# Optimization experiments

Hardware: AMD Instinct MI355X
Metric: run time of the kernel (lower is better)

## Reference

```python
import jax, jax.numpy as jnp
import numpy as np

G = 8          # GroupNorm groups
EPS = 1e-5
L = 4          # num_layers
C = 64         # hidden_channels
CIN = 2        # in_channels


def group_norm(x, gamma, beta):
    B, Cc, H, W = x.shape
    xr = x.reshape(B, G, Cc // G, H, W)
    mu = xr.mean(axis=(2, 3, 4), keepdims=True)
    var = xr.var(axis=(2, 3, 4), keepdims=True)
    xn = ((xr - mu) * jax.lax.rsqrt(var + EPS)).reshape(B, Cc, H, W)
    return xn * gamma[:, None, None] + beta[:, None, None]


def conv1x1(x, w, b):
    # x: [B,Ci,H,W], w: [Co,Ci] -> [B,Co,H,W]
    return jnp.einsum('bchw,oc->bohw', x, w) + b[None, :, None, None]


def conv3x3(x, w, b):
    y = jax.lax.conv_general_dilated(x, w, (1, 1), 'SAME',
                                     dimension_numbers=('NCHW', 'OIHW', 'NCHW'))
    return y + b[None, :, None, None]


def setup_inputs() -> dict:
    key = jax.random.key(0)
    ks = jax.random.split(key, 20)
    s = 0.05
    inp = {
        'x': jax.random.normal(ks[0], (2, CIN, 256, 256), jnp.float32),
        'hidden': jnp.zeros((2, L, C, C), jnp.float32),
        'W_in': jax.random.normal(ks[1], (C, CIN, 3, 3), jnp.float32) * s,
        'b_in': jnp.zeros((C,), jnp.float32),
        'gamma': jnp.ones((L, C), jnp.float32),
        'beta': jnp.zeros((L, C), jnp.float32),
        'Wq': jax.random.normal(ks[2], (L, C, C), jnp.float32) * s,
        'bq': jnp.zeros((L, C), jnp.float32),
        'Wk': jax.random.normal(ks[3], (L, C, C), jnp.float32) * s,
        'bk': jnp.zeros((L, C), jnp.float32),
        'Wv': jax.random.normal(ks[4], (L, C, C), jnp.float32) * s,
        'bv': jnp.zeros((L, C), jnp.float32),
        'Wg': jax.random.normal(ks[5], (L, 2 * C, C), jnp.float32) * s,
        'bg': jnp.zeros((L, 2 * C), jnp.float32),
        'Wp': jax.random.normal(ks[6], (L, C, C), jnp.float32) * s,
        'bp': jnp.zeros((L, C), jnp.float32),
        'W_out': jax.random.normal(ks[7], (CIN, C, 3, 3), jnp.float32) * s,
        'b_out': jnp.zeros((CIN,), jnp.float32),
    }
    return inp


def gla_layer(feat, prev_mem, gamma, beta, Wq, bq, Wk, bk, Wv, bv, Wg, bg, Wp, bp):
    B, Cc, H, W = feat.shape
    N = H * W
    scale = Cc ** (-0.5)
    xn = group_norm(feat, gamma, beta)
    q = conv1x1(xn, Wq, bq).reshape(B, Cc, N) * scale
    k = conv1x1(xn, Wk, bk).reshape(B, Cc, N)
    v = conv1x1(xn, Wv, bv).reshape(B, Cc, N)
    gates = conv1x1(xn, Wg, bg).reshape(B, 2 * Cc, N)
    f_gate = jax.nn.sigmoid(gates[:, :Cc])
    i_gate = jax.nn.sigmoid(gates[:, Cc:])
    k_gated = k * i_gate
    new_knowledge = jnp.einsum('bcn,bdn->bcd', k_gated, v) / N  # [B,C,C]
    global_forget = f_gate.mean(axis=2)[:, :, None]              # [B,C,1]
    new_mem = global_forget * prev_mem + new_knowledge
    retrieved = jnp.einsum('bcn,bcd->bdn', q, new_mem).reshape(B, Cc, H, W)
    out = conv1x1(retrieved, Wp, bp) + feat
    return out, new_mem


def reference(x, hidden, W_in, b_in, gamma, beta, Wq, bq, Wk, bk, Wv, bv,
              Wg, bg, Wp, bp, W_out, b_out):
    feat = conv3x3(x, W_in, b_in)
    mems = []
    for i in range(L):
        feat, m = gla_layer(feat, hidden[:, i], gamma[i], beta[i],
                            Wq[i], bq[i], Wk[i], bk[i], Wv[i], bv[i],
                            Wg[i], bg[i], Wp[i], bp[i])
        mems.append(m)
    new_hidden = jnp.stack(mems, axis=1)  # [B,L,C,C]
    out = conv3x3(feat, W_out, b_out) + x
    return out, new_hidden
```

## Files before the change

kernel.cpp:

```cpp
#include <hip/hip_runtime.h>
#include <hip/hip_bf16.h>

typedef __hip_bfloat16 bf16;
typedef __attribute__((ext_vector_type(8))) short bf16x8;
typedef __attribute__((ext_vector_type(4))) short short4v;
typedef __attribute__((ext_vector_type(4))) float f32x4;

#define BATCH 2
#define CH 64
#define NPIX 65536
#define HDIM 256
#define NLAYER 4
#define NGRP 8
#define NSLOT 512

#define OFS_FEAT   0ull
#define OFS_KSLOT  33554432ull
#define OFS_MEMBG  50331648ull
#define OFS_FSUM   50348032ull
#define OFS_SSUM   50364416ull
#define OFS_BEFF   50380800ull
#define OFS_MEFFB  50381312ull
#define OFS_WKB    50397696ull
#define OFS_WVB    50430464ull
#define OFS_WGB    50463232ull
#define OFS_WTOUT  50528768ull
#define OFS_WPB    50533376ull
#define OFS_WQTB   50566144ull
#define ZERO_BYTES 32768

__device__ __forceinline__ float sigmoidf_(float x){ return 1.0f/(1.0f+__expf(-x)); }

__device__ __forceinline__ short f2bs(float x){
  unsigned u = __float_as_uint(x);
  u += 0x7fffu + ((u >> 16) & 1u);
  return (short)(u >> 16);
}

__device__ __forceinline__ float waveReduce(float v){
  #pragma unroll
  for (int off=32; off; off>>=1) v += __shfl_xor(v, off, 64);
  return v;
}

__global__ void k_prepw(const float* __restrict__ Wk, const float* __restrict__ Wv,
                        const float* __restrict__ Wg, const float* __restrict__ Wout,
                        const float* __restrict__ Wp, const float* __restrict__ Wq,
                        short* __restrict__ Wkb, short* __restrict__ Wvb,
                        short* __restrict__ Wgb, float* __restrict__ wtout,
                        short* __restrict__ Wpb, short* __restrict__ Wqtb){
  int i = blockIdx.x*256 + threadIdx.x;
  if (i < 16384){
    Wkb[i] = f2bs(Wk[i]);
    Wvb[i] = f2bs(Wv[i]);
    Wpb[i] = f2bs(Wp[i]);
    int l = i >> 12, within = i & 4095;
    int e = within >> 6, c = within & 63;
    Wqtb[i] = f2bs(Wq[l*4096 + c*64 + e]);
  }
  if (i < 32768) Wgb[i] = f2bs(Wg[i]);
  if (i < 1152){
    int o = i / 576, rem = i % 576;
    int k = rem >> 6, c = rem & 63;
    wtout[(o*9 + k)*64 + c] = Wout[o*576 + c*9 + k];
  }
}

__device__ __forceinline__ void blockStats(const float* gs, const float* gq,
                                           float* ssum_b, int t){
  __shared__ float sacc[16];
  if (t < 16) sacc[t] = 0.f;
  __syncthreads();
  #pragma unroll
  for (int g=0; g<NGRP; g++){
    float s  = waveReduce(gs[g]);
    float sq = waveReduce(gq[g]);
    if ((t & 63) == 0){ atomicAdd(&sacc[g*2], s); atomicAdd(&sacc[g*2+1], sq); }
  }
  __syncthreads();
  if (t < 16) atomicAdd(&ssum_b[t*32], sacc[t]);
}

__global__ void k_conv_in(const float* __restrict__ x, const float* __restrict__ w,
                          const float* __restrict__ bias,
                          float* __restrict__ feat, float* __restrict__ ssum){
  int b = blockIdx.y;
  int t = threadIdx.x;
  int n = blockIdx.x*256 + t;
  int y = n >> 8, xx = n & 255;
  float patch[18];
  int idx = 0;
  #pragma unroll
  for (int ci=0; ci<2; ci++)
    #pragma unroll
    for (int dy=-1; dy<=1; dy++)
      #pragma unroll
      for (int dx=-1; dx<=1; dx++){
        int yy = y+dy, xc = xx+dx;
        float v = 0.f;
        if (yy>=0 && yy<HDIM && xc>=0 && xc<HDIM)
          v = x[((b*2+ci)*HDIM + yy)*HDIM + xc];
        patch[idx++] = v;
      }
  float gs[NGRP], gq[NGRP];
  #pragma unroll
  for (int g=0; g<NGRP; g++){ gs[g]=0.f; gq[g]=0.f; }
  float* fb = feat + ((size_t)b*NPIX + n)*64;
  #pragma unroll
  for (int c4=0; c4<16; c4++){
    f32x4 ov;
    #pragma unroll
    for (int j=0;j<4;j++){
      int o = c4*4 + j;
      float acc = bias[o];
      #pragma unroll
      for (int k=0; k<18; k++) acc += w[o*18+k]*patch[k];
      ov[j] = acc;
      gs[o>>3] += acc; gq[o>>3] += acc*acc;
    }
    *(f32x4*)(fb + c4*4) = ov;
  }
  blockStats(gs, gq, ssum + b*512, t);
}

__device__ __forceinline__ void gnCoef(const float* __restrict__ ssum_l, int b, int t,
                                       const float* __restrict__ gammaP,
                                       const float* __restrict__ betaP, int l,
                                       float* s_gnA, float* s_gnB){
  if (t < 64){
    int g = t >> 3;
    const float inv = 1.0f/(8.0f*NPIX);
    float s  = ssum_l[(b*16 + g*2)*32];
    float sq = ssum_l[(b*16 + g*2 + 1)*32];
    float mu = s*inv;
    float var = sq*inv - mu*mu;
    float rstd = rsqrtf(var + 1e-5f);
    float A = rstd * gammaP[l*64 + t];
    s_gnA[t] = A;
    s_gnB[t] = betaP[l*64 + t] - mu * A;
  }
}

__global__ __launch_bounds__(256,3) void k_qkvg_know(
    const float* __restrict__ feat, const float* __restrict__ ssum_l,
    const float* __restrict__ gammaP, const float* __restrict__ betaP,
    const short* __restrict__ Wkb, const float* __restrict__ bkP,
    const short* __restrict__ Wvb, const float* __restrict__ bvP,
    const short* __restrict__ Wgb, const float* __restrict__ bgP,
    int l, float* __restrict__ kslot, float* __restrict__ f_sum)
{
  int b = blockIdx.y;
  int n0 = blockIdx.x * 128;
  int t = threadIdx.x;
  int w = t >> 6;
  int lane = t & 63;
  int m = lane & 15;
  int quad = lane >> 4;
  int rowbase = w*16;

  __shared__ short s_buf[17408];
  short* s_kg = s_buf;
  short* s_v  = s_buf + 8704;
  short* s_xn = s_buf;
  __shared__ float s_gnA[64], s_gnB[64];

  gnCoef(ssum_l, b, t, gammaP, betaP, l, s_gnA, s_gnB);

  float bkv[4], biv[4], bvv[4], bfv[4], fs[4];
  #pragma unroll
  for (int r=0;r<4;r++){
    int row = rowbase + quad*4 + r;
    bkv[r] = bkP[l*64 + row];
    biv[r] = bgP[l*128 + 64 + row];
    bvv[r] = bvP[l*64 + row];
    bfv[r] = bgP[l*128 + row];
    fs[r] = 0.f;
  }
  f32x4 z4 = {0.f,0.f,0.f,0.f};
  f32x4 accn[4];
  #pragma unroll
  for (int dt=0;dt<4;dt++) accn[dt] = z4;

  __syncthreads();

  const float* fbase = feat + ((size_t)b*NPIX + n0)*64;
  #pragma unroll
  for (int i=0;i<8;i++){
    int chunk = t + i*256;
    int px = chunk >> 4, cq = chunk & 15;
    f32x4 fv = *(const f32x4*)(fbase + px*64 + cq*4);
    short4v xs;
    #pragma unroll
    for (int j=0;j<4;j++)
      xs[j] = f2bs(fmaf(fv[j], s_gnA[cq*4+j], s_gnB[cq*4+j]));
    *(short4v*)&s_xn[px*72 + cq*4] = xs;
  }
  __syncthreads();

  bf16x8 Bf[2][8];
  #pragma unroll
  for (int kc=0;kc<2;kc++)
    #pragma unroll
    for (int nt=0;nt<8;nt++)
      Bf[kc][nt] = *(const bf16x8*)&s_xn[(nt*16+m)*72 + kc*32 + quad*8];
  __syncthreads();

  {
    bf16x8 Ak[2], Ai[2];
    #pragma unroll
    for (int kc=0;kc<2;kc++){
      Ak[kc] = *(const bf16x8*)&Wkb[l*4096 + (rowbase+m)*64 + kc*32 + quad*8];
      Ai[kc] = *(const bf16x8*)&Wgb[l*8192 + (64+rowbase+m)*64 + kc*32 + quad*8];
    }
    #pragma unroll
    for (int half=0; half<2; half++){
      f32x4 acck[4], acci[4];
      #pragma unroll
      for (int q4=0;q4<4;q4++){ acck[q4]=z4; acci[q4]=z4; }
      #pragma unroll
      for (int kc=0;kc<2;kc++)
        #pragma unroll
        for (int q4=0;q4<4;q4++){
          acck[q4] = __builtin_amdgcn_mfma_f32_16x16x32_bf16(Ak[kc], Bf[kc][half*4+q4], acck[q4], 0,0,0);
          acci[q4] = __builtin_amdgcn_mfma_f32_16x16x32_bf16(Ai[kc], Bf[kc][half*4+q4], acci[q4], 0,0,0);
        }
      #pragma unroll
      for (int q4=0;q4<4;q4++){
        int nt = half*4+q4;
        #pragma unroll
        for (int r=0;r<4;r++){
          int row = rowbase + quad*4 + r;
          float kv = acck[q4][r] + bkv[r];
          float iv = acci[q4][r] + biv[r];
          s_kg[row*136 + nt*16 + m] = f2bs(kv * sigmoidf_(iv));
        }
      }
    }
  }
  {
    bf16x8 Av[2];
    #pragma unroll
    for (int kc=0;kc<2;kc++)
      Av[kc] = *(const bf16x8*)&Wvb[l*4096 + (rowbase+m)*64 + kc*32 + quad*8];
    #pragma unroll
    for (int half=0; half<2; half++){
      f32x4 accv[4];
      #pragma unroll
      for (int q4=0;q4<4;q4++) accv[q4]=z4;
      #pragma unroll
      for (int kc=0;kc<2;kc++)
        #pragma unroll
        for (int q4=0;q4<4;q4++)
          accv[q4] = __builtin_amdgcn_mfma_f32_16x16x32_bf16(Av[kc], Bf[kc][half*4+q4], accv[q4], 0,0,0);
      #pragma unroll
      for (int q4=0;q4<4;q4++){
        int nt = half*4+q4;
        #pragma unroll
        for (int r=0;r<4;r++){
          int row = rowbase + quad*4 + r;
          s_v[row*136 + nt*16 + m] = f2bs(accv[q4][r] + bvv[r]);
        }
      }
    }
  }
  {
    bf16x8 Af[2];
    #pragma unroll
    for (int kc=0;kc<2;kc++)
      Af[kc] = *(const bf16x8*)&Wgb[l*8192 + (rowbase+m)*64 + kc*32 + quad*8];
    #pragma unroll
    for (int half=0; half<2; half++){
      f32x4 accf[4];
      #pragma unroll
      for (int q4=0;q4<4;q4++) accf[q4]=z4;
      #pragma unroll
      for (int kc=0;kc<2;kc++)
        #pragma unroll
        for (int q4=0;q4<4;q4++)
          accf[q4] = __builtin_amdgcn_mfma_f32_16x16x32_bf16(Af[kc], Bf[kc][half*4+q4], accf[q4], 0,0,0);
      #pragma unroll
      for (int q4=0;q4<4;q4++)
        #pragma unroll
        for (int r=0;r<4;r++)
          fs[r] += sigmoidf_(accf[q4][r] + bfv[r]);
    }
  }
  __syncthreads();

  #pragma unroll
  for (int kc4=0; kc4<4; kc4++){
    bf16x8 a = *(const bf16x8*)&s_kg[(rowbase + m)*136 + kc4*32 + quad*8];
    #pragma unroll
    for (int dt=0; dt<4; dt++){
      bf16x8 bv8 = *(const bf16x8*)&s_v[(dt*16 + m)*136 + kc4*32 + quad*8];
      accn[dt] = __builtin_amdgcn_mfma_f32_16x16x32_bf16(a, bv8, accn[dt], 0,0,0);
    }
  }

  #pragma unroll
  for (int off=1; off<16; off<<=1)
    #pragma unroll
    for (int r=0;r<4;r++) fs[r] += __shfl_xor(fs[r], off, 64);
  if (m == 0){
    #pragma unroll
    for (int r=0;r<4;r++)
      atomicAdd(&f_sum[(b*64 + rowbase + quad*4 + r)*32], fs[r]);
  }
  float* kr = kslot + ((size_t)b*NSLOT + blockIdx.x)*4096;
  #pragma unroll
  for (int dt=0;dt<4;dt++)
    #pragma unroll
    for (int r=0;r<4;r++)
      kr[(rowbase + quad*4 + r)*64 + dt*16 + m] = accn[dt][r];
}

__global__ __launch_bounds__(256) void k_memreduce(
    const float* __restrict__ kslot, const float* __restrict__ f_sum,
    const float* __restrict__ hidden_in, int l,
    float* __restrict__ hidden_out, short* __restrict__ membG)
{
  int b = blockIdx.y;
  int t = threadIdx.x;
  int e = t & 127;
  int half = t >> 7;
  int cd = blockIdx.x*128 + e;

  const float* base = kslot + ((size_t)b*NSLOT + half*256)*4096 + cd;
  float s = 0.f;
  #pragma unroll 16
  for (int sl=0; sl<256; sl++) s += base[(size_t)sl*4096];

  __shared__ float red[128];
  if (half) red[e] = s;
  __syncthreads();
  if (!half){
    const float invN = 1.0f/(float)NPIX;
    float kn = (s + red[e]) * invN;
    float fmean = f_sum[(b*64 + (cd>>6))*32] * invN;
    float pm = hidden_in[(size_t)(b*NLAYER+l)*4096 + cd];
    float nm = fmean*pm + kn;
    hidden_out[(size_t)(b*NLAYER+l)*4096 + cd] = nm;
    membG[b*4096 + cd] = f2bs(nm);
  }
}

__global__ __launch_bounds__(256) void k_meff(
    const short* __restrict__ membG, float* __restrict__ f_sum,
    const short* __restrict__ Wpb, const short* __restrict__ Wqtb,
    const float* __restrict__ bqP, const float* __restrict__ bpP,
    int l, short* __restrict__ Meffb, float* __restrict__ beff,
    float* __restrict__ ssum_next)
{
  int b = blockIdx.x;
  int t = threadIdx.x;
  int w = t >> 6;
  int lane = t & 63;
  int m = lane & 15;
  int quad = lane >> 4;

  __shared__ short s_memb[64*72];
  __shared__ short s_mfb[64*72];
  __shared__ float s_bq[64];

  if (t < 64) s_bq[t] = bqP[l*64 + t];

  #pragma unroll
  for (int i=0;i<16;i++){
    int cd = t + i*256;
    int c = cd >> 6, d = cd & 63;
    s_memb[c*72 + d] = membG[b*4096 + cd];
  }
  __syncthreads();
  if (t < 64) f_sum[(b*64 + t)*32] = 0.f;
  if (t < 16) ssum_next[(b*16 + t)*32] = 0.f;

  f32x4 z4 = {0.f,0.f,0.f,0.f};

  bf16x8 Ap[2];
  #pragma unroll
  for (int kc=0;kc<2;kc++)
    Ap[kc] = *(const bf16x8*)&Wpb[l*4096 + (w*16+m)*64 + kc*32 + quad*8];

  float be[4];
  #pragma unroll
  for (int r=0;r<4;r++) be[r] = 0.f;

  #pragma unroll
  for (int ct=0; ct<4; ct++){
    f32x4 a = z4;
    #pragma unroll
    for (int kc=0;kc<2;kc++){
      bf16x8 Bm = *(const bf16x8*)&s_memb[(ct*16+m)*72 + kc*32 + quad*8];
      a = __builtin_amdgcn_mfma_f32_16x16x32_bf16(Ap[kc], Bm, a, 0,0,0);
    }
    int c = ct*16 + m;
    #pragma unroll
    for (int r=0;r<4;r++){
      int o = w*16 + quad*4 + r;
      s_mfb[o*72 + c] = f2bs(a[r]);
      be[r] += a[r] * s_bq[c];
    }
  }
  #pragma unroll
  for (int off=1; off<16; off<<=1)
    #pragma unroll
    for (int r=0;r<4;r++) be[r] += __shfl_xor(be[r], off, 64);
  if (m == 0){
    #pragma unroll
    for (int r=0;r<4;r++){
      int o = w*16 + quad*4 + r;
      beff[b*64 + o] = bpP[l*64 + o] + 0.125f*be[r];
    }
  }
  __syncthreads();

  bf16x8 Am2[2];
  #pragma unroll
  for (int kc=0;kc<2;kc++)
    Am2[kc] = *(const bf16x8*)&s_mfb[(w*16+m)*72 + kc*32 + quad*8];
  #pragma unroll
  for (int et=0; et<4; et++){
    f32x4 a = z4;
    #pragma unroll
    for (int kc=0;kc<2;kc++){
      bf16x8 Bq = *(const bf16x8*)&Wqtb[l*4096 + (et*16+m)*64 + kc*32 + quad*8];
      a = __builtin_amdgcn_mfma_f32_16x16x32_bf16(Am2[kc], Bq, a, 0,0,0);
    }
    #pragma unroll
    for (int r=0;r<4;r++){
      int o = w*16 + quad*4 + r;
      Meffb[(size_t)b*4096 + o*64 + et*16 + m] = f2bs(0.125f*a[r]);
    }
  }
}

__global__ __launch_bounds__(256,3) void k_retrproj(
    const float* __restrict__ ssum_l,
    const float* __restrict__ gammaP, const float* __restrict__ betaP,
    const short* __restrict__ Meffb, const float* __restrict__ beff,
    int l, float* __restrict__ feat, float* __restrict__ ssum_next)
{
  int b = blockIdx.y;
  int n0 = blockIdx.x * 128;
  int t = threadIdx.x;
  int w = t >> 6;
  int lane = t & 63;
  int m = lane & 15;
  int quad = lane >> 4;

  __shared__ float s_out[128*68];
  short* s_xn = (short*)s_out;
  __shared__ float s_gnA[64], s_gnB[64], s_beff[64];
  __shared__ float s_sacc[16];

  gnCoef(ssum_l, b, t, gammaP, betaP, l, s_gnA, s_gnB);
  if (t < 64) s_beff[t] = beff[b*64 + t];
  if (t < 16) s_sacc[t] = 0.f;
  __syncthreads();

  const float* fbase = feat + ((size_t)b*NPIX + n0)*64;
  #pragma unroll
  for (int i=0;i<8;i++){
    int chunk = t + i*256;
    int px = chunk >> 4, cq = chunk & 15;
    f32x4 fv = *(const f32x4*)(fbase + px*64 + cq*4);
    short4v xs;
    #pragma unroll
    for (int j=0;j<4;j++)
      xs[j] = f2bs(fmaf(fv[j], s_gnA[cq*4+j], s_gnB[cq*4+j]));
    *(short4v*)&s_xn[px*72 + cq*4] = xs;
  }
  __syncthreads();

  bf16x8 Bf[2][8];
  #pragma unroll
  for (int kc=0;kc<2;kc++)
    #pragma unroll
    for (int nt=0;nt<8;nt++)
      Bf[kc][nt] = *(const bf16x8*)&s_xn[(nt*16+m)*72 + kc*32 + quad*8];

  bf16x8 Am[2];
  #pragma unroll
  for (int kc=0;kc<2;kc++)
    Am[kc] = *(const bf16x8*)&Meffb[(size_t)b*4096 + (w*16 + m)*64 + kc*32 + quad*8];
  __syncthreads();

  f32x4 acc[8];
  f32x4 z4 = {0.f,0.f,0.f,0.f};
  #pragma unroll
  for (int nt=0;nt<8;nt++) acc[nt]=z4;
  #pragma unroll
  for (int kc=0;kc<2;kc++)
    #pragma unroll
    for (int nt=0;nt<8;nt++)
      acc[nt] = __builtin_amdgcn_mfma_f32_16x16x32_bf16(Am[kc], Bf[kc][nt], acc[nt], 0,0,0);

  #pragma unroll
  for (int nt=0;nt<8;nt++)
    #pragma unroll
    for (int r=0;r<4;r++)
      s_out[(nt*16+m)*68 + w*16 + quad*4 + r] = acc[nt][r];
  __syncthreads();

  float gsv = 0.f, gqv = 0.f;
  int cq = t & 15;
  #pragma unroll
  for (int i=0;i<8;i++){
    int chunk = t + i*256;
    int px = chunk >> 4;
    float* fp = (float*)(fbase + px*64 + cq*4);
    f32x4 fv = *(const f32x4*)fp;
    f32x4 ov = *(const f32x4*)&s_out[px*68 + cq*4];
    f32x4 res;
    #pragma unroll
    for (int j=0;j<4;j++){
      float o = fv[j] + ov[j] + s_beff[cq*4+j];
      res[j] = o;
      gsv += o; gqv += o*o;
    }
    *(f32x4*)fp = res;
  }
  gsv += __shfl_xor(gsv, 1, 64);  gqv += __shfl_xor(gqv, 1, 64);
  gsv += __shfl_xor(gsv, 16, 64); gqv += __shfl_xor(gqv, 16, 64);
  gsv += __shfl_xor(gsv, 32, 64); gqv += __shfl_xor(gqv, 32, 64);
  if ((lane & 49) == 0){
    int g = (lane & 15) >> 1;
    atomicAdd(&s_sacc[g*2], gsv);
    atomicAdd(&s_sacc[g*2+1], gqv);
  }
  __syncthreads();
  if (t < 16) atomicAdd(&ssum_next[(b*16 + t)*32], s_sacc[t]);
}

__global__ void k_conv_out(const float* __restrict__ feat, const float* __restrict__ wt,
                           const float* __restrict__ bias,
                           const float* __restrict__ xin, float* __restrict__ out){
  int b = blockIdx.y;
  int y = blockIdx.x;
  int xx = threadIdx.x;
  float acc0 = bias[0], acc1 = bias[1];
  #pragma unroll
  for (int dy=-1; dy<=1; dy++){
    int yy = y + dy;
    if (yy < 0 || yy >= HDIM) continue;
    #pragma unroll
    for (int dx=-1; dx<=1; dx++){
      int xc = xx + dx;
      if (xc >= 0 && xc < HDIM){
        const float* fp = feat + ((size_t)b*NPIX + yy*HDIM + xc)*64;
        const float* w0 = wt + ((0*3 + dy+1)*3 + dx+1)*64;
        const float* w1 = wt + ((1*3 + dy+1)*3 + dx+1)*64;
        #pragma unroll
        for (int c4=0;c4<16;c4++){
          f32x4 fv  = *(const f32x4*)(fp + c4*4);
          f32x4 wv0 = *(const f32x4*)(w0 + c4*4);
          f32x4 wv1 = *(const f32x4*)(w1 + c4*4);
          #pragma unroll
          for (int j=0;j<4;j++){
            acc0 += fv[j]*wv0[j];
            acc1 += fv[j]*wv1[j];
          }
        }
      }
    }
  }
  size_t p0 = (size_t)(b*2+0)*NPIX + y*HDIM + xx;
  size_t p1 = (size_t)(b*2+1)*NPIX + y*HDIM + xx;
  out[p0] = acc0 + xin[p0];
  out[p1] = acc1 + xin[p1];
}

extern "C" void kernel_launch(void* const* d_in, const int* in_sizes, int n_in,
                              void* d_out, int out_size, void* d_ws, size_t ws_size,
                              hipStream_t stream){
  char* ws = (char*)d_ws;
  float* feat  = (float*)(ws + OFS_FEAT);
  float* kslot = (float*)(ws + OFS_KSLOT);
  short* membg = (short*)(ws + OFS_MEMBG);
  float* fsum  = (float*)(ws + OFS_FSUM);
  float* ssum  = (float*)(ws + OFS_SSUM);
  float* beff  = (float*)(ws + OFS_BEFF);
  short* meffb = (short*)(ws + OFS_MEFFB);
  short* wkb   = (short*)(ws + OFS_WKB);
  short* wvb   = (short*)(ws + OFS_WVB);
  short* wgb   = (short*)(ws + OFS_WGB);
  float* wtout = (float*)(ws + OFS_WTOUT);
  short* wpb   = (short*)(ws + OFS_WPB);
  short* wqtb  = (short*)(ws + OFS_WQTB);

  const float* x      = (const float*)d_in[0];
  const float* hidden = (const float*)d_in[1];
  const float* W_in   = (const float*)d_in[2];
  const float* b_in   = (const float*)d_in[3];
  const float* gamma  = (const float*)d_in[4];
  const float* beta   = (const float*)d_in[5];
  const float* Wq     = (const float*)d_in[6];
  const float* bq     = (const float*)d_in[7];
  const float* Wk     = (const float*)d_in[8];
  const float* bk     = (const float*)d_in[9];
  const float* Wv     = (const float*)d_in[10];
  const float* bv     = (const float*)d_in[11];
  const float* Wg     = (const float*)d_in[12];
  const float* bg     = (const float*)d_in[13];
  const float* Wp     = (const float*)d_in[14];
  const float* bp     = (const float*)d_in[15];
  const float* W_out  = (const float*)d_in[16];
  const float* b_out  = (const float*)d_in[17];

  float* out        = (float*)d_out;
  float* hidden_out = out + BATCH*2*NPIX;

  hipMemsetAsync(ws + OFS_FSUM, 0, ZERO_BYTES, stream);
  k_prepw<<<dim3(128), dim3(256), 0, stream>>>(Wk, Wv, Wg, W_out, Wp, Wq,
                                               wkb, wvb, wgb, wtout, wpb, wqtb);
  k_conv_in<<<dim3(HDIM, BATCH), dim3(256), 0, stream>>>(x, W_in, b_in, feat, ssum);

  for (int l=0; l<NLAYER; l++){
    float* ssum_l = ssum + (l & 1)*1024;
    float* ssum_n = ssum + ((l+1) & 1)*1024;
    k_qkvg_know<<<dim3(NPIX/128, BATCH), dim3(256), 0, stream>>>(
        feat, ssum_l, gamma, beta, wkb, bk, wvb, bv, wgb, bg, l, kslot, fsum);
    k_memreduce<<<dim3(32, BATCH), dim3(256), 0, stream>>>(
        kslot, fsum, hidden, l, hidden_out, membg);
    k_meff<<<dim3(BATCH), dim3(256), 0, stream>>>(
        membg, fsum, wpb, wqtb, bq, bp, l, meffb, beff, ssum_n);
    k_retrproj<<<dim3(NPIX/128, BATCH), dim3(256), 0, stream>>>(
        ssum_l, gamma, beta, meffb, beff, l, feat, ssum_n);
  }

  k_conv_out<<<dim3(HDIM, BATCH), dim3(256), 0, stream>>>(feat, wtout, b_out, x, out);
}
```

Baseline: 393.0 us.

## Store per-block knowledge partials as bf16 and fuse memreduce with meff

Per-block C×C knowledge partials are now written as bf16 instead of fp32, which halves the scratch traffic between the projection kernel and the reduction. The reduction and the effective-matrix kernels are merged into one launch. An atomic counter per layer and batch lets the last-finishing block do the Meff computation. This removes one kernel launch per layer and the traffic cost of the partials, at the price of bf16 rounding in the partial sums and reliance on a threadfence and counter pattern.

Result: slower. 409.9 us (+4.3%).

```diff
diff --git a/kernel.cpp b/kernel.cpp
--- a/kernel.cpp
+++ b/kernel.cpp
@@ -16,18 +16,19 @@
 
 #define OFS_FEAT   0ull
 #define OFS_KSLOT  33554432ull
-#define OFS_MEMBG  50331648ull
-#define OFS_FSUM   50348032ull
-#define OFS_SSUM   50364416ull
-#define OFS_BEFF   50380800ull
-#define OFS_MEFFB  50381312ull
-#define OFS_WKB    50397696ull
-#define OFS_WVB    50430464ull
-#define OFS_WGB    50463232ull
-#define OFS_WTOUT  50528768ull
-#define OFS_WPB    50533376ull
-#define OFS_WQTB   50566144ull
-#define ZERO_BYTES 32768
+#define OFS_MEMBG  41943040ull
+#define OFS_FSUM   41959424ull
+#define OFS_SSUM   41975808ull
+#define OFS_CNT    41992192ull
+#define OFS_BEFF   41992704ull
+#define OFS_MEFFB  41993216ull
+#define OFS_WKB    42009600ull
+#define OFS_WVB    42042368ull
+#define OFS_WGB    42075136ull
+#define OFS_WTOUT  42140672ull
+#define OFS_WPB    42145280ull
+#define OFS_WQTB   42178048ull
+#define ZERO_BYTES 33280
 
 __device__ __forceinline__ float sigmoidf_(float x){ return 1.0f/(1.0f+__expf(-x)); }
 
@@ -35,6 +36,9 @@
   unsigned u = __float_as_uint(x);
   u += 0x7fffu + ((u >> 16) & 1u);
   return (short)(u >> 16);
+}
+__device__ __forceinline__ float bs2f(short x){
+  return __uint_as_float(((unsigned)(unsigned short)x) << 16);
 }
 
 __device__ __forceinline__ float waveReduce(float v){
@@ -147,7 +151,7 @@
     const short* __restrict__ Wkb, const float* __restrict__ bkP,
     const short* __restrict__ Wvb, const float* __restrict__ bvP,
     const short* __restrict__ Wgb, const float* __restrict__ bgP,
-    int l, float* __restrict__ kslot, float* __restrict__ f_sum)
+    int l, short* __restrict__ kslot, float* __restrict__ f_sum)
 {
   int b = blockIdx.y;
   int n0 = blockIdx.x * 128;
@@ -306,18 +310,22 @@
     for (int r=0;r<4;r++)
       atomicAdd(&f_sum[(b*64 + rowbase + quad*4 + r)*32], fs[r]);
   }
-  float* kr = kslot + ((size_t)b*NSLOT + blockIdx.x)*4096;
+  short* kr = kslot + ((size_t)b*NSLOT + blockIdx.x)*4096;
   #pragma unroll
   for (int dt=0;dt<4;dt++)
     #pragma unroll
     for (int r=0;r<4;r++)
-      kr[(rowbase + quad*4 + r)*64 + dt*16 + m] = accn[dt][r];
-}
-
-__global__ __launch_bounds__(256) void k_memreduce(
-    const float* __restrict__ kslot, const float* __restrict__ f_sum,
-    const float* __restrict__ hidden_in, int l,
-    float* __restrict__ hidden_out, short* __restrict__ membG)
+      kr[(rowbase + quad*4 + r)*64 + dt*16 + m] = f2bs(accn[dt][r]);
+}
+
+__global__ __launch_bounds__(256) void k_memupd(
+    const short* __restrict__ kslot, float* __restrict__ f_sum,
+    const float* __restrict__ hidden_in,
+    const short* __restrict__ Wpb, const short* __restrict__ Wqtb,
+    const float* __restrict__ bqP, const float* __restrict__ bpP,
+    int l, float* __restrict__ hidden_out, short* __restrict__ membG,
+    short* __restrict__ Meffb, float* __restrict__ beff,
+    float* __restrict__ ssum_next, unsigned* __restrict__ cnt)
 {
   int b = blockIdx.y;
   int t = threadIdx.x;
@@ -325,34 +333,33 @@
   int half = t >> 7;
   int cd = blockIdx.x*128 + e;
 
-  const float* base = kslot + ((size_t)b*NSLOT + half*256)*4096 + cd;
-  float s = 0.f;
-  #pragma unroll 16
-  for (int sl=0; sl<256; sl++) s += base[(size_t)sl*4096];
-
   __shared__ float red[128];
-  if (half) red[e] = s;
-  __syncthreads();
-  if (!half){
-    const float invN = 1.0f/(float)NPIX;
-    float kn = (s + red[e]) * invN;
-    float fmean = f_sum[(b*64 + (cd>>6))*32] * invN;
-    float pm = hidden_in[(size_t)(b*NLAYER+l)*4096 + cd];
-    float nm = fmean*pm + kn;
-    hidden_out[(size_t)(b*NLAYER+l)*4096 + cd] = nm;
-    membG[b*4096 + cd] = f2bs(nm);
-  }
-}
-
-__global__ __launch_bounds__(256) void k_meff(
-    const short* __restrict__ membG, float* __restrict__ f_sum,
-    const short* __restrict__ Wpb, const short* __restrict__ Wqtb,
-    const float* __restrict__ bqP, const float* __restrict__ bpP,
-    int l, short* __restrict__ Meffb, float* __restrict__ beff,
-    float* __restrict__ ssum_next)
-{
-  int b = blockIdx.x;
-  int t = threadIdx.x;
+  __shared__ unsigned s_done;
+
+  {
+    const short* base = kslot + ((size_t)b*NSLOT + half*256)*4096 + cd;
+    float s = 0.f;
+    #pragma unroll 16
+    for (int sl=0; sl<256; sl++) s += bs2f(base[(size_t)sl*4096]);
+    if (half) red[e] = s;
+    __syncthreads();
+    if (!half){
+      const float invN = 1.0f/(float)NPIX;
+      float kn = (s + red[e]) * invN;
+      float fmean = f_sum[(b*64 + (cd>>6))*32] * invN;
+      float pm = hidden_in[(size_t)(b*NLAYER+l)*4096 + cd];
+      float nm = fmean*pm + kn;
+      hidden_out[(size_t)(b*NLAYER+l)*4096 + cd] = nm;
+      membG[b*4096 + cd] = f2bs(nm);
+    }
+  }
+  __syncthreads();
+  __threadfence();
+  if (t == 0) s_done = atomicAdd(&cnt[l*2 + b], 1u);
+  __syncthreads();
+  if (s_done != gridDim.x - 1) return;
+  __threadfence();
+
   int w = t >> 6;
   int lane = t & 63;
   int m = lane & 15;
@@ -362,17 +369,19 @@
   __shared__ short s_mfb[64*72];
   __shared__ float s_bq[64];
 
-  if (t < 64) s_bq[t] = bqP[l*64 + t];
+  if (t < 64){
+    s_bq[t] = bqP[l*64 + t];
+    f_sum[(b*64 + t)*32] = 0.f;
+  }
+  if (t < 16) ssum_next[(b*16 + t)*32] = 0.f;
 
   #pragma unroll
   for (int i=0;i<16;i++){
-    int cd = t + i*256;
-    int c = cd >> 6, d = cd & 63;
-    s_memb[c*72 + d] = membG[b*4096 + cd];
-  }
-  __syncthreads();
-  if (t < 64) f_sum[(b*64 + t)*32] = 0.f;
-  if (t < 16) ssum_next[(b*16 + t)*32] = 0.f;
+    int cd2 = t + i*256;
+    int c = cd2 >> 6, d = cd2 & 63;
+    s_memb[c*72 + d] = membG[b*4096 + cd2];
+  }
+  __syncthreads();
 
   f32x4 z4 = {0.f,0.f,0.f,0.f};
 
@@ -575,10 +584,11 @@
                               hipStream_t stream){
   char* ws = (char*)d_ws;
   float* feat  = (float*)(ws + OFS_FEAT);
-  float* kslot = (float*)(ws + OFS_KSLOT);
+  short* kslot = (short*)(ws + OFS_KSLOT);
   short* membg = (short*)(ws + OFS_MEMBG);
   float* fsum  = (float*)(ws + OFS_FSUM);
   float* ssum  = (float*)(ws + OFS_SSUM);
+  unsigned* cnt = (unsigned*)(ws + OFS_CNT);
   float* beff  = (float*)(ws + OFS_BEFF);
   short* meffb = (short*)(ws + OFS_MEFFB);
   short* wkb   = (short*)(ws + OFS_WKB);
@@ -620,10 +630,9 @@
     float* ssum_n = ssum + ((l+1) & 1)*1024;
     k_qkvg_know<<<dim3(NPIX/128, BATCH), dim3(256), 0, stream>>>(
         feat, ssum_l, gamma, beta, wkb, bk, wvb, bv, wgb, bg, l, kslot, fsum);
-    k_memreduce<<<dim3(32, BATCH), dim3(256), 0, stream>>>(
-        kslot, fsum, hidden, l, hidden_out, membg);
-    k_meff<<<dim3(BATCH), dim3(256), 0, stream>>>(
-        membg, fsum, wpb, wqtb, bq, bp, l, meffb, beff, ssum_n);
+    k_memupd<<<dim3(32, BATCH), dim3(256), 0, stream>>>(
+        kslot, fsum, hidden, wpb, wqtb, bq, bp, l, hidden_out, membg,
+        meffb, beff, ssum_n, cnt);
     k_retrproj<<<dim3(NPIX/128, BATCH), dim3(256), 0, stream>>>(
         ssum_l, gamma, beta, meffb, beff, l, feat, ssum_n);
   }
```

## Store residual feature map and knowledge partial slots in bf16

Applied to the files above, without the earlier changes.

Changes the persistent feature tensor and the per-block knowledge partial sums from fp32 to bf16 storage, halving global memory traffic across every layer kernel, the conv_out stencil, and the memreduce pass. Loads become 8-wide bf16 vectors that are converted to fp32 for arithmetic, and the workspace offsets shrink to match. The risk is accuracy: the residual stream accumulates bf16 rounding across four layers, and the partial knowledge matrices lose precision before the reduction.

Result: faster. 358.1 us (-8.9%).

```diff
diff --git a/kernel.cpp b/kernel.cpp
--- a/kernel.cpp
+++ b/kernel.cpp
@@ -15,18 +15,18 @@
 #define NSLOT 512
 
 #define OFS_FEAT   0ull
-#define OFS_KSLOT  33554432ull
-#define OFS_MEMBG  50331648ull
-#define OFS_FSUM   50348032ull
-#define OFS_SSUM   50364416ull
-#define OFS_BEFF   50380800ull
-#define OFS_MEFFB  50381312ull
-#define OFS_WKB    50397696ull
-#define OFS_WVB    50430464ull
-#define OFS_WGB    50463232ull
-#define OFS_WTOUT  50528768ull
-#define OFS_WPB    50533376ull
-#define OFS_WQTB   50566144ull
+#define OFS_KSLOT  16777216ull
+#define OFS_MEMBG  25165824ull
+#define OFS_FSUM   25182208ull
+#define OFS_SSUM   25198592ull
+#define OFS_BEFF   25214976ull
+#define OFS_MEFFB  25215488ull
+#define OFS_WKB    25231872ull
+#define OFS_WVB    25264640ull
+#define OFS_WGB    25297408ull
+#define OFS_WTOUT  25362944ull
+#define OFS_WPB    25367552ull
+#define OFS_WQTB   25400320ull
 #define ZERO_BYTES 32768
 
 __device__ __forceinline__ float sigmoidf_(float x){ return 1.0f/(1.0f+__expf(-x)); }
@@ -35,6 +35,9 @@
   unsigned u = __float_as_uint(x);
   u += 0x7fffu + ((u >> 16) & 1u);
   return (short)(u >> 16);
+}
+__device__ __forceinline__ float bs2f(short x){
+  return __uint_as_float(((unsigned)(unsigned short)x) << 16);
 }
 
 __device__ __forceinline__ float waveReduce(float v){
@@ -83,7 +86,7 @@
 
 __global__ void k_conv_in(const float* __restrict__ x, const float* __restrict__ w,
                           const float* __restrict__ bias,
-                          float* __restrict__ feat, float* __restrict__ ssum){
+                          short* __restrict__ feat, float* __restrict__ ssum){
   int b = blockIdx.y;
   int t = threadIdx.x;
   int n = blockIdx.x*256 + t;
@@ -105,20 +108,20 @@
   float gs[NGRP], gq[NGRP];
   #pragma unroll
   for (int g=0; g<NGRP; g++){ gs[g]=0.f; gq[g]=0.f; }
-  float* fb = feat + ((size_t)b*NPIX + n)*64;
+  short* fb = feat + ((size_t)b*NPIX + n)*64;
   #pragma unroll
   for (int c4=0; c4<16; c4++){
-    f32x4 ov;
+    short4v sv;
     #pragma unroll
     for (int j=0;j<4;j++){
       int o = c4*4 + j;
       float acc = bias[o];
       #pragma unroll
       for (int k=0; k<18; k++) acc += w[o*18+k]*patch[k];
-      ov[j] = acc;
+      sv[j] = f2bs(acc);
       gs[o>>3] += acc; gq[o>>3] += acc*acc;
     }
-    *(f32x4*)(fb + c4*4) = ov;
+    *(short4v*)(fb + c4*4) = sv;
   }
   blockStats(gs, gq, ssum + b*512, t);
 }
@@ -142,12 +145,12 @@
 }
 
 __global__ __launch_bounds__(256,3) void k_qkvg_know(
-    const float* __restrict__ feat, const float* __restrict__ ssum_l,
+    const short* __restrict__ feat, const float* __restrict__ ssum_l,
     const float* __restrict__ gammaP, const float* __restrict__ betaP,
     const short* __restrict__ Wkb, const float* __restrict__ bkP,
     const short* __restrict__ Wvb, const float* __restrict__ bvP,
     const short* __restrict__ Wgb, const float* __restrict__ bgP,
-    int l, float* __restrict__ kslot, float* __restrict__ f_sum)
+    int l, short* __restrict__ kslot, float* __restrict__ f_sum)
 {
   int b = blockIdx.y;
   int n0 = blockIdx.x * 128;
@@ -183,17 +186,21 @@
 
   __syncthreads();
 
-  const float* fbase = feat + ((size_t)b*NPIX + n0)*64;
-  #pragma unroll
-  for (int i=0;i<8;i++){
+  const short* fbase = feat + ((size_t)b*NPIX + n0)*64;
+  #pragma unroll
+  for (int i=0;i<4;i++){
     int chunk = t + i*256;
-    int px = chunk >> 4, cq = chunk & 15;
-    f32x4 fv = *(const f32x4*)(fbase + px*64 + cq*4);
-    short4v xs;
+    int px = chunk >> 3, c8 = (chunk & 7)*8;
+    bf16x8 rv = *(const bf16x8*)(fbase + px*64 + c8);
+    short4v lo, hi;
     #pragma unroll
     for (int j=0;j<4;j++)
-      xs[j] = f2bs(fmaf(fv[j], s_gnA[cq*4+j], s_gnB[cq*4+j]));
-    *(short4v*)&s_xn[px*72 + cq*4] = xs;
+      lo[j] = f2bs(fmaf(bs2f(rv[j]), s_gnA[c8+j], s_gnB[c8+j]));
+    #pragma unroll
+    for (int j=0;j<4;j++)
+      hi[j] = f2bs(fmaf(bs2f(rv[j+4]), s_gnA[c8+4+j], s_gnB[c8+4+j]));
+    *(short4v*)&s_xn[px*72 + c8]     = lo;
+    *(short4v*)&s_xn[px*72 + c8 + 4] = hi;
   }
   __syncthreads();
 
@@ -306,16 +313,16 @@
     for (int r=0;r<4;r++)
       atomicAdd(&f_sum[(b*64 + rowbase + quad*4 + r)*32], fs[r]);
   }
-  float* kr = kslot + ((size_t)b*NSLOT + blockIdx.x)*4096;
+  short* kr = kslot + ((size_t)b*NSLOT + blockIdx.x)*4096;
   #pragma unroll
   for (int dt=0;dt<4;dt++)
     #pragma unroll
     for (int r=0;r<4;r++)
-      kr[(rowbase + quad*4 + r)*64 + dt*16 + m] = accn[dt][r];
+      kr[(rowbase + quad*4 + r)*64 + dt*16 + m] = f2bs(accn[dt][r]);
 }
 
 __global__ __launch_bounds__(256) void k_memreduce(
-    const float* __restrict__ kslot, const float* __restrict__ f_sum,
+    const short* __restrict__ kslot, const float* __restrict__ f_sum,
     const float* __restrict__ hidden_in, int l,
     float* __restrict__ hidden_out, short* __restrict__ membG)
 {
@@ -325,10 +332,10 @@
   int half = t >> 7;
   int cd = blockIdx.x*128 + e;
 
-  const float* base = kslot + ((size_t)b*NSLOT + half*256)*4096 + cd;
+  const short* base = kslot + ((size_t)b*NSLOT + half*256)*4096 + cd;
   float s = 0.f;
   #pragma unroll 16
-  for (int sl=0; sl<256; sl++) s += base[(size_t)sl*4096];
+  for (int sl=0; sl<256; sl++) s += bs2f(base[(size_t)sl*4096]);
 
   __shared__ float red[128];
   if (half) red[e] = s;
@@ -438,7 +445,7 @@
     const float* __restrict__ ssum_l,
     const float* __restrict__ gammaP, const float* __restrict__ betaP,
     const short* __restrict__ Meffb, const float* __restrict__ beff,
-    int l, float* __restrict__ feat, float* __restrict__ ssum_next)
+    int l, short* __restrict__ feat, float* __restrict__ ssum_next)
 {
   int b = blockIdx.y;
   int n0 = blockIdx.x * 128;
@@ -458,17 +465,21 @@
   if (t < 16) s_sacc[t] = 0.f;
   __syncthreads();
 
-  const float* fbase = feat + ((size_t)b*NPIX + n0)*64;
-  #pragma unroll
-  for (int i=0;i<8;i++){
+  short* fbase = feat + ((size_t)b*NPIX + n0)*64;
+  #pragma unroll
+  for (int i=0;i<4;i++){
     int chunk = t + i*256;
-    int px = chunk >> 4, cq = chunk & 15;
-    f32x4 fv = *(const f32x4*)(fbase + px*64 + cq*4);
-    short4v xs;
+    int px = chunk >> 3, c8 = (chunk & 7)*8;
+    bf16x8 rv = *(const bf16x8*)(fbase + px*64 + c8);
+    short4v lo, hi;
     #pragma unroll
     for (int j=0;j<4;j++)
-      xs[j] = f2bs(fmaf(fv[j], s_gnA[cq*4+j], s_gnB[cq*4+j]));
-    *(short4v*)&s_xn[px*72 + cq*4] = xs;
+      lo[j] = f2bs(fmaf(bs2f(rv[j]), s_gnA[c8+j], s_gnB[c8+j]));
+    #pragma unroll
+    for (int j=0;j<4;j++)
+      hi[j] = f2bs(fmaf(bs2f(rv[j+4]), s_gnA[c8+4+j], s_gnB[c8+4+j]));
+    *(short4v*)&s_xn[px*72 + c8]     = lo;
+    *(short4v*)&s_xn[px*72 + c8 + 4] = hi;
   }
   __syncthreads();
 
@@ -503,28 +514,36 @@
   __syncthreads();
 
   float gsv = 0.f, gqv = 0.f;
-  int cq = t & 15;
-  #pragma unroll
-  for (int i=0;i<8;i++){
+  int c8 = (t & 7)*8;
+  #pragma unroll
+  for (int i=0;i<4;i++){
     int chunk = t + i*256;
-    int px = chunk >> 4;
-    float* fp = (float*)(fbase + px*64 + cq*4);
-    f32x4 fv = *(const f32x4*)fp;
-    f32x4 ov = *(const f32x4*)&s_out[px*68 + cq*4];
-    f32x4 res;
+    int px = chunk >> 3;
+    short* fp = fbase + px*64 + c8;
+    bf16x8 rv = *(const bf16x8*)fp;
+    f32x4 o1 = *(const f32x4*)&s_out[px*68 + c8];
+    f32x4 o2 = *(const f32x4*)&s_out[px*68 + c8 + 4];
+    short4v r1, r2;
     #pragma unroll
     for (int j=0;j<4;j++){
-      float o = fv[j] + ov[j] + s_beff[cq*4+j];
-      res[j] = o;
+      float o = bs2f(rv[j]) + o1[j] + s_beff[c8+j];
+      r1[j] = f2bs(o);
       gsv += o; gqv += o*o;
     }
-    *(f32x4*)fp = res;
-  }
-  gsv += __shfl_xor(gsv, 1, 64);  gqv += __shfl_xor(gqv, 1, 64);
+    #pragma unroll
+    for (int j=0;j<4;j++){
+      float o = bs2f(rv[j+4]) + o2[j] + s_beff[c8+4+j];
+      r2[j] = f2bs(o);
+      gsv += o; gqv += o*o;
+    }
+    *(short4v*)fp = r1;
+    *(short4v*)(fp+4) = r2;
+  }
+  gsv += __shfl_xor(gsv, 8, 64);  gqv += __shfl_xor(gqv, 8, 64);
   gsv += __shfl_xor(gsv, 16, 64); gqv += __shfl_xor(gqv, 16, 64);
   gsv += __shfl_xor(gsv, 32, 64); gqv += __shfl_xor(gqv, 32, 64);
-  if ((lane & 49) == 0){
-    int g = (lane & 15) >> 1;
+  if ((lane & 56) == 0){
+    int g = lane & 7;
     atomicAdd(&s_sacc[g*2], gsv);
     atomicAdd(&s_sacc[g*2+1], gqv);
   }
@@ -532,7 +551,7 @@
   if (t < 16) atomicAdd(&ssum_next[(b*16 + t)*32], s_sacc[t]);
 }
 
-__global__ void k_conv_out(const float* __restrict__ feat, const float* __restrict__ wt,
+__global__ void k_conv_out(const short* __restrict__ feat, const float* __restrict__ wt,
                            const float* __restrict__ bias,
                            const float* __restrict__ xin, float* __restrict__ out){
   int b = blockIdx.y;
@@ -547,18 +566,21 @@
     for (int dx=-1; dx<=1; dx++){
       int xc = xx + dx;
       if (xc >= 0 && xc < HDIM){
-        const float* fp = feat + ((size_t)b*NPIX + yy*HDIM + xc)*64;
+        const short* fp = feat + ((size_t)b*NPIX + yy*HDIM + xc)*64;
         const float* w0 = wt + ((0*3 + dy+1)*3 + dx+1)*64;
         const float* w1 = wt + ((1*3 + dy+1)*3 + dx+1)*64;
         #pragma unroll
-        for (int c4=0;c4<16;c4++){
-          f32x4 fv  = *(const f32x4*)(fp + c4*4);
-          f32x4 wv0 = *(const f32x4*)(w0 + c4*4);
-          f32x4 wv1 = *(const f32x4*)(w1 + c4*4);
+        for (int c8=0;c8<8;c8++){
+          bf16x8 fv = *(const bf16x8*)(fp + c8*8);
+          f32x4 w0a = *(const f32x4*)(w0 + c8*8);
+          f32x4 w0b = *(const f32x4*)(w0 + c8*8 + 4);
+          f32x4 w1a = *(const f32x4*)(w1 + c8*8);
+          f32x4 w1b = *(const f32x4*)(w1 + c8*8 + 4);
           #pragma unroll
           for (int j=0;j<4;j++){
-            acc0 += fv[j]*wv0[j];
-            acc1 += fv[j]*wv1[j];
+            float fa = bs2f(fv[j]), fb2 = bs2f(fv[j+4]);
+            acc0 += fa*w0a[j] + fb2*w0b[j];
+            acc1 += fa*w1a[j] + fb2*w1b[j];
           }
         }
       }
@@ -574,8 +596,8 @@
                               void* d_out, int out_size, void* d_ws, size_t ws_size,
                               hipStream_t stream){
   char* ws = (char*)d_ws;
-  float* feat  = (float*)(ws + OFS_FEAT);
-  float* kslot = (float*)(ws + OFS_KSLOT);
+  short* feat  = (short*)(ws + OFS_FEAT);
+  short* kslot = (short*)(ws + OFS_KSLOT);
   short* membg = (short*)(ws + OFS_MEMBG);
   float* fsum  = (float*)(ws + OFS_FSUM);
   float* ssum  = (float*)(ws + OFS_SSUM);
```
